# Optimization experiments

Hardware: AMD Instinct MI355X
Metric: run time of the kernel (lower is better)

Reference implementation:

```python
import jax, jax.numpy as jnp
import numpy as np

# Transformer-XL relative multi-head attention (eval mode, dropout = identity)
B, Q, M, D, H = 2, 1024, 1024, 1024, 16
DH = D // H          # 64 head dim
K = Q + M            # key length = memory + current segment
SCALE = 0.02         # param init scale


def setup_inputs() -> dict:
    key = jax.random.key(0)
    ks = jax.random.split(key, 10)
    return {
        "inputs": jax.random.normal(ks[0], (B, Q, D), jnp.float32),
        "inputs_mem": jax.random.normal(ks[1], (B, M, D), jnp.float32),
        "r": jax.random.normal(ks[2], (B, K, D), jnp.float32),
        "W_qkv": jax.random.normal(ks[3], (D, 3 * D), jnp.float32) * SCALE,
        "b_qkv": jnp.zeros((3 * D,), jnp.float32),
        "W_r": jax.random.normal(ks[4], (D, D), jnp.float32) * SCALE,
        "b_r": jnp.zeros((D,), jnp.float32),
        "W_o": jax.random.normal(ks[5], (D, D), jnp.float32) * SCALE,
        "b_o": jnp.zeros((D,), jnp.float32),
        "u": jax.random.normal(ks[6], (1, H, 1, DH), jnp.float32) * SCALE,
        "v": jax.random.normal(ks[7], (1, H, 1, DH), jnp.float32) * SCALE,
    }


def _split_heads(x):
    # [B, L, D] -> [B, H, L, DH]
    b, l, _ = x.shape
    return x.reshape(b, l, H, DH).transpose(0, 2, 1, 3)


def _rel_shift(x):
    # Transformer-XL relative shift: pad one zero column on the left,
    # reshape to [B, H, K+1, Q], drop first row, reshape back.
    b, h, q, k = x.shape
    x = jnp.pad(x, ((0, 0), (0, 0), (0, 0), (1, 0)))
    x = x.reshape(b, h, k + 1, q)[:, :, 1:, :]
    return x.reshape(b, h, q, k)


def reference(inputs, inputs_mem, r, W_qkv, b_qkv, W_r, b_r, W_o, b_o, u, v):
    cat = jnp.concatenate([inputs_mem, inputs], axis=1)      # [B, K, D]
    w = cat @ W_qkv + b_qkv                                   # [B, K, 3D]
    rp = r @ W_r + b_r                                        # [B, K, D]
    # NOTE: source splits as (q, v, k) in that order
    w_q, w_v, w_k = jnp.split(w, 3, axis=-1)
    hq = _split_heads(w_q)[:, :, -Q:]                          # [B, H, Q, DH]
    hk = _split_heads(w_k)                                     # [B, H, K, DH]
    hv = _split_heads(w_v)                                     # [B, H, K, DH]
    hr = _split_heads(rp)                                      # [B, H, K, DH]
    ac = jnp.einsum('bhqd,bhkd->bhqk', hq + u, hk)             # content term
    bd = _rel_shift(jnp.einsum('bhqd,bhkd->bhqk', hq + v, hr)) # position term
    score = (ac + bd) / (DH ** 0.5)
    # causal mask with memory: query i attends to all mem + positions <= i
    mem_len = K - Q
    mask = (jnp.arange(K)[None, :] <= mem_len + jnp.arange(Q)[:, None]).astype(jnp.float32)
    score = score * mask - 1e30 * (1.0 - mask)
    weights = jax.nn.softmax(score, axis=-1)                   # [B, H, Q, K]
    out = jnp.einsum('bhqk,bhkd->bhqd', weights, hv)           # [B, H, Q, DH]
    out = out.transpose(0, 2, 1, 3).reshape(B, Q, D)
    return out @ W_o + b_o
```

## Files before the change

kernel.cpp:

```cpp
#include <hip/hip_runtime.h>
#include <hip/hip_bf16.h>
#include <stdint.h>


typedef __bf16 bf16;
typedef __bf16 bf16x2 __attribute__((ext_vector_type(2)));
typedef __bf16 bf16x4 __attribute__((ext_vector_type(4)));
typedef __bf16 bf16x8 __attribute__((ext_vector_type(8)));
typedef float  f32x4  __attribute__((ext_vector_type(4)));

__device__ __forceinline__ void async_copy16(void* lds, const void* g) {
    auto gp = (const __attribute__((address_space(1))) void*)(uintptr_t)g;
    auto lp = (__attribute__((address_space(3))) void*)(uint32_t)(uintptr_t)lds;
    __builtin_amdgcn_global_load_lds(gp, lp, 16, 0, 0);
}

__device__ __forceinline__ void gemm128_core(
    const bf16* __restrict__ A, const bf16* __restrict__ Bt, const int Kd,
    const int m0, const int n0, bf16* As, bf16* Bs, f32x4 acc[4][4])
{
    const int tid  = threadIdx.x;
    const int lane = tid & 63;
    const int wave = tid >> 6;
    const int wr   = (wave >> 1) * 64;
    const int wc   = (wave & 1) * 64;
    const int lr   = lane & 15;
    const int q4   = lane >> 4;

#pragma unroll
    for (int i = 0; i < 4; ++i)
#pragma unroll
        for (int j = 0; j < 4; ++j) {
            acc[i][j][0] = 0.f; acc[i][j][1] = 0.f; acc[i][j][2] = 0.f; acc[i][j][3] = 0.f;
        }

    auto stage = [&](int buf, int k0) {
#pragma unroll
        for (int it = 0; it < 2; ++it) {
            const int cb0   = (it * 4 + wave) * 64;
            const int chunk = cb0 + lane;
            const int row   = chunk >> 2;
            const int cg    = (chunk & 3) * 8;
            async_copy16(As + buf * 4096 + cb0 * 8, A  + (size_t)(m0 + row) * Kd + k0 + cg);
            async_copy16(Bs + buf * 4096 + cb0 * 8, Bt + (size_t)(n0 + row) * Kd + k0 + cg);
        }
    };

    const int NT = Kd >> 5;
    stage(0, 0);
    __syncthreads();

    for (int t = 0; t < NT; ++t) {
        const int buf = t & 1;
        if (t + 1 < NT) stage(buf ^ 1, (t + 1) * 32);

        const bf16* Ab = As + buf * 4096;
        const bf16* Bb = Bs + buf * 4096;
        bf16x8 af[4], bfr[4];
#pragma unroll
        for (int rb = 0; rb < 4; ++rb)
            af[rb] = *(const bf16x8*)&Ab[(wr + rb * 16 + lr) * 32 + q4 * 8];
#pragma unroll
        for (int cb = 0; cb < 4; ++cb)
            bfr[cb] = *(const bf16x8*)&Bb[(wc + cb * 16 + lr) * 32 + q4 * 8];
#pragma unroll
        for (int rb = 0; rb < 4; ++rb)
#pragma unroll
            for (int cb = 0; cb < 4; ++cb)
                acc[rb][cb] = __builtin_amdgcn_mfma_f32_16x16x32_bf16(af[rb], bfr[cb], acc[rb][cb], 0, 0, 0);
        __syncthreads();
    }
}

__device__ __forceinline__ void gemm64_core(
    const bf16* __restrict__ A, const bf16* __restrict__ Bt, const int Kd,
    const int m0, const int n0, bf16* As, bf16* Bs, f32x4 acc[2][4])
{
    const int tid  = threadIdx.x;
    const int lane = tid & 63;
    const int wave = tid >> 6;
    const int wr   = (wave >> 1) * 32;
    const int wc   = (wave & 1) * 64;
    const int lr   = lane & 15;
    const int q4   = lane >> 4;

#pragma unroll
    for (int i = 0; i < 2; ++i)
#pragma unroll
        for (int j = 0; j < 4; ++j) {
            acc[i][j][0] = 0.f; acc[i][j][1] = 0.f; acc[i][j][2] = 0.f; acc[i][j][3] = 0.f;
        }

    auto stage = [&](int buf, int k0) {
        {
            const int chunk = tid;
            const int row   = chunk >> 2;
            const int cg    = (chunk & 3) * 8;
            async_copy16(As + buf * 2048 + (wave * 64) * 8, A + (size_t)(m0 + row) * Kd + k0 + cg);
        }
#pragma unroll
        for (int it = 0; it < 2; ++it) {
            const int cb0   = (it * 4 + wave) * 64;
            const int chunk = cb0 + lane;
            const int row   = chunk >> 2;
            const int cg    = (chunk & 3) * 8;
            async_copy16(Bs + buf * 4096 + cb0 * 8, Bt + (size_t)(n0 + row) * Kd + k0 + cg);
        }
    };

    const int NT = Kd >> 5;
    stage(0, 0);
    __syncthreads();

    for (int t = 0; t < NT; ++t) {
        const int buf = t & 1;
        if (t + 1 < NT) stage(buf ^ 1, (t + 1) * 32);

        const bf16* Ab = As + buf * 2048;
        const bf16* Bb = Bs + buf * 4096;
        bf16x8 af[2], bfr[4];
#pragma unroll
        for (int rb = 0; rb < 2; ++rb)
            af[rb] = *(const bf16x8*)&Ab[(wr + rb * 16 + lr) * 32 + q4 * 8];
#pragma unroll
        for (int cb = 0; cb < 4; ++cb)
            bfr[cb] = *(const bf16x8*)&Bb[(wc + cb * 16 + lr) * 32 + q4 * 8];
#pragma unroll
        for (int rb = 0; rb < 2; ++rb)
#pragma unroll
            for (int cb = 0; cb < 4; ++cb)
                acc[rb][cb] = __builtin_amdgcn_mfma_f32_16x16x32_bf16(af[rb], bfr[cb], acc[rb][cb], 0, 0, 0);
        __syncthreads();
    }
}

__global__ __launch_bounds__(256) void k_prep(
    const float* __restrict__ Wqkv, const float* __restrict__ Wr,
    const float* __restrict__ Wo,
    const float* __restrict__ mem, const float* __restrict__ inp,
    const float* __restrict__ r,
    bf16* __restrict__ Wqkvt, bf16* __restrict__ Wrt, bf16* __restrict__ Wot,
    bf16* __restrict__ catb, bf16* __restrict__ rb)
{
    __shared__ float t[32][33];
    int id = blockIdx.x;
    if (id < 5120) {
        const float* in; bf16* out; int C, bx, by;
        if (id < 3072)      { in = Wqkv; out = Wqkvt; C = 3072; bx = id % 96; by = id / 96; }
        else if (id < 4096) { id -= 3072; in = Wr; out = Wrt; C = 1024; bx = id & 31; by = id >> 5; }
        else                { id -= 4096; in = Wo; out = Wot; C = 1024; bx = id & 31; by = id >> 5; }
        const int R = 1024;
        const int c0 = bx * 32, r0 = by * 32;
        const int lc = threadIdx.x & 31, lrow = threadIdx.x >> 5;
#pragma unroll
        for (int p = 0; p < 4; ++p)
            t[lrow + p * 8][lc] = in[(size_t)(r0 + lrow + p * 8) * C + c0 + lc];
        __syncthreads();
#pragma unroll
        for (int p = 0; p < 4; ++p)
            out[(size_t)(c0 + lrow + p * 8) * R + r0 + lc] = (bf16)t[lc][lrow + p * 8];
    } else if (id < 9216) {
        const int e   = ((id - 5120) * 256 + threadIdx.x) * 4;
        const int row = e >> 10, dc = e & 1023;
        const int b   = row >> 11, k = row & 2047;
        const float* src = (k < 1024) ? mem + ((size_t)b * 1024 + k) * 1024 + dc
                                      : inp + ((size_t)b * 1024 + (k - 1024)) * 1024 + dc;
        float4 f = *(const float4*)src;
        bf16x4 o; o[0] = (bf16)f.x; o[1] = (bf16)f.y; o[2] = (bf16)f.z; o[3] = (bf16)f.w;
        *(bf16x4*)&catb[e] = o;
    } else {
        const int e = ((id - 9216) * 256 + threadIdx.x) * 4;
        float4 f = *(const float4*)(r + e);
        bf16x4 o; o[0] = (bf16)f.x; o[1] = (bf16)f.y; o[2] = (bf16)f.z; o[3] = (bf16)f.w;
        *(bf16x4*)&rb[e] = o;
    }
}

__global__ __launch_bounds__(256) void k_gemm_qkvr(
    const bf16* __restrict__ catb, const bf16* __restrict__ Wqkvt,
    const float* __restrict__ b_qkv, const float* __restrict__ u, const float* __restrict__ v,
    const bf16* __restrict__ rb_, const bf16* __restrict__ Wrt,
    const float* __restrict__ b_r,
    bf16* __restrict__ hq_u, bf16* __restrict__ hq_v,
    bf16* __restrict__ hk, bf16* __restrict__ hvT, bf16* __restrict__ hr)
{
    __shared__ bf16 lds[4 * 128 * 32];
    f32x4 acc[4][4];
    const int lane = threadIdx.x & 63, wave = threadIdx.x >> 6;
    const int wr = (wave >> 1) * 64, wc = (wave & 1) * 64;
    const int lr = lane & 15, q4 = lane >> 4;
    const int y = blockIdx.y;

    if (y < 16) {
        const int m0 = blockIdx.x * 128;
        const int n0 = 1024 + y * 128;
        gemm128_core(catb, Wqkvt, 1024, m0, n0, lds, lds + 2 * 4096, acc);
#pragma unroll
        for (int rb = 0; rb < 4; ++rb) {
#pragma unroll
            for (int cb = 0; cb < 4; ++cb) {
                const int col  = n0 + wc + cb * 16 + lr;
                const int part = col >> 10;
                const int hd   = col & 1023;
                const int h    = hd >> 6, d = hd & 63;
                const float bcol = b_qkv[col];
#pragma unroll
                for (int r = 0; r < 4; ++r) {
                    const int row = m0 + wr + rb * 16 + q4 * 4 + r;
                    const int b   = row >> 11, k = row & 2047;
                    const float val = acc[rb][cb][r] + bcol;
                    if (part == 1) {
                        const int ks = (k & ~63) | ((k & 63) ^ ((d & 7) << 3));
                        hvT[(((size_t)(b * 16 + h)) * 64 + d) * 2048 + ks] = (bf16)val;
                    } else {
                        const int ds = d ^ ((k & 7) << 3);
                        hk[(((size_t)(b * 16 + h)) * 2048 + k) * 64 + ds] = (bf16)val;
                    }
                }
            }
        }
    } else if (y < 20) {
        const int linear = (y - 16) * 32 + blockIdx.x;
        const int n0 = (linear & 7) * 128;
        const int mi = linear >> 3;
        const int m0 = (mi >> 3) * 2048 + 1024 + (mi & 7) * 128;
        gemm128_core(catb, Wqkvt, 1024, m0, n0, lds, lds + 2 * 4096, acc);
#pragma unroll
        for (int rb = 0; rb < 4; ++rb) {
#pragma unroll
            for (int cb = 0; cb < 4; ++cb) {
                const int col = n0 + wc + cb * 16 + lr;
                const int h = col >> 6, d = col & 63;
                const float bcol = b_qkv[col];
                const float uc = u[col], vc = v[col];
#pragma unroll
                for (int r = 0; r < 4; ++r) {
                    const int row = m0 + wr + rb * 16 + q4 * 4 + r;
                    const int b   = row >> 11, k = row & 2047;
                    const float val = acc[rb][cb][r] + bcol;
                    const size_t o = (((size_t)(b * 16 + h)) * 1024 + (k - 1024)) * 64 + d;
                    hq_u[o] = (bf16)(val + uc);
                    hq_v[o] = (bf16)(val + vc);
                }
            }
        }
    } else {
        const int m0 = blockIdx.x * 128;
        const int n0 = (y - 20) * 128;
        gemm128_core(rb_, Wrt, 1024, m0, n0, lds, lds + 2 * 4096, acc);
#pragma unroll
        for (int rb = 0; rb < 4; ++rb) {
#pragma unroll
            for (int cb = 0; cb < 4; ++cb) {
                const int col = n0 + wc + cb * 16 + lr;
                const int h = col >> 6, d = col & 63;
                const float bcol = b_r[col];
#pragma unroll
                for (int r = 0; r < 4; ++r) {
                    const int row = m0 + wr + rb * 16 + q4 * 4 + r;
                    const int b = row >> 11, k = row & 2047;
                    const int ds = d ^ ((k & 7) << 3);
                    hr[(((size_t)(b * 16 + h)) * 2048 + k) * 64 + ds] = (bf16)(acc[rb][cb][r] + bcol);
                }
            }
        }
    }
}

__global__ __launch_bounds__(256) void k_gemm_out(
    const bf16* __restrict__ attn, const bf16* __restrict__ Wt,
    const float* __restrict__ bias, float* __restrict__ out)
{
    __shared__ bf16 lds[2 * 2048 + 2 * 4096];
    f32x4 acc[2][4];
    const int m0 = blockIdx.x * 64, n0 = blockIdx.y * 128;
    gemm64_core(attn, Wt, 1024, m0, n0, lds, lds + 2 * 2048, acc);

    const int lane = threadIdx.x & 63, wave = threadIdx.x >> 6;
    const int wr = (wave >> 1) * 32, wc = (wave & 1) * 64;
    const int lr = lane & 15, q4 = lane >> 4;
#pragma unroll
    for (int rb = 0; rb < 2; ++rb) {
#pragma unroll
        for (int cb = 0; cb < 4; ++cb) {
            const int col = n0 + wc + cb * 16 + lr;
            const float bcol = bias[col];
#pragma unroll
            for (int r = 0; r < 4; ++r) {
                const int row = m0 + wr + rb * 16 + q4 * 4 + r;
                out[(size_t)row * 1024 + col] = acc[rb][cb][r] + bcol;
            }
        }
    }
}

__global__ __launch_bounds__(256) void k_attn(
    const bf16* __restrict__ hq_u, const bf16* __restrict__ hq_v,
    const bf16* __restrict__ hk, const bf16* __restrict__ hvT,
    const bf16* __restrict__ hr, bf16* __restrict__ attn)
{
    __shared__ bf16 Ks[2][64][64];
    __shared__ bf16 Vt[2][64][64];
    __shared__ bf16 Rs[192][64];
    __shared__ bf16 U[4][1600];

    const int bh = blockIdx.y;
    const int qt = (bh & 16) ? (15 - (int)blockIdx.x) : (int)blockIdx.x;
    const int q0 = qt * 64;
    const int tid = threadIdx.x, lane = tid & 63, wave = tid >> 6;
    const int lr = lane & 15, q4 = lane >> 4;
    bf16* Uw = &U[wave][0];

    const int nt  = 17 + qt;
    const int m0c = 15 - qt;
    const size_t kvbase = (size_t)bh * 2048 * 64;

    const int r0_ = tid >> 3, c0_ = (tid & 7) * 8;
    const int r1_ = 32 + r0_, c1_ = c0_;

    auto stage_kv = [&](int t, int buf) {
        const int k0 = t * 64;
        async_copy16(&Ks[buf][r0_][c0_], &hk [kvbase + (size_t)(k0 + r0_) * 64 + c0_]);
        async_copy16(&Ks[buf][r1_][c1_], &hk [kvbase + (size_t)(k0 + r1_) * 64 + c1_]);
        async_copy16(&Vt[buf][r0_][c0_], &hvT[kvbase + (size_t)r0_ * 2048 + k0 + c0_]);
        async_copy16(&Vt[buf][r1_][c1_], &hvT[kvbase + (size_t)r1_ * 2048 + k0 + c1_]);
    };
    auto stage_r = [&](int c, int slot) {
        if (c * 64 < 2048) {
            async_copy16(&Rs[slot * 64 + r0_][c0_], &hr[kvbase + (size_t)(c * 64 + r0_) * 64 + c0_]);
            async_copy16(&Rs[slot * 64 + r1_][c1_], &hr[kvbase + (size_t)(c * 64 + r1_) * 64 + c1_]);
        }
    };

    const size_t qrow = ((size_t)bh * 1024 + q0 + wave * 16 + lr) * 64;
    const bf16x8 qu0 = *(const bf16x8*)&hq_u[qrow + q4 * 8];
    const bf16x8 qu1 = *(const bf16x8*)&hq_u[qrow + 32 + q4 * 8];
    const bf16x8 qv0 = *(const bf16x8*)&hq_v[qrow + q4 * 8];
    const bf16x8 qv1 = *(const bf16x8*)&hq_v[qrow + 32 + q4 * 8];

    const int sw  = (lr & 7) << 3;
    const int cA0 = (q4 * 8) ^ sw;
    const int cA1 = (32 + q4 * 8) ^ sw;

    f32x4 Oacc[4];
#pragma unroll
    for (int i = 0; i < 4; ++i) { Oacc[i][0] = 0.f; Oacc[i][1] = 0.f; Oacc[i][2] = 0.f; Oacc[i][3] = 0.f; }
    float lp[4] = {0.f, 0.f, 0.f, 0.f};

    stage_kv(0, 0);
    stage_r(m0c,     m0c % 3);
    stage_r(m0c + 1, (m0c + 1) % 3);
    __syncthreads();

    for (int t = 0; t < nt; ++t) {
        const int k0  = t * 64;
        const int mt  = m0c + t;
        const int s0  = mt % 3;
        const int s1  = (s0 + 1 == 3) ? 0 : s0 + 1;
        const int s2  = (s1 + 1 == 3) ? 0 : s1 + 1;
        const int buf = t & 1;
        const bool more = (t + 1 < nt);
        if (more) { stage_kv(t + 1, buf ^ 1); stage_r(mt + 2, s2); }

        __builtin_amdgcn_s_setprio(1);
        f32x4 S[4];
#pragma unroll
        for (int cb = 0; cb < 4; ++cb) {
            const bf16x8 kf0 = *(const bf16x8*)&Ks[buf][cb * 16 + lr][cA0];
            const bf16x8 kf1 = *(const bf16x8*)&Ks[buf][cb * 16 + lr][cA1];
            f32x4 z; z[0] = 0.f; z[1] = 0.f; z[2] = 0.f; z[3] = 0.f;
            z = __builtin_amdgcn_mfma_f32_16x16x32_bf16(qu0, kf0, z, 0, 0, 0);
            S[cb] = __builtin_amdgcn_mfma_f32_16x16x32_bf16(qu1, kf1, z, 0, 0, 0);
        }
#pragma unroll
        for (int jbi = 0; jbi < 5; ++jbi) {
            const int jb   = jbi + 3 - wave;
            const int rrow = ((jb & 4) ? s1 : s0) * 64 + (jb & 3) * 16 + lr;
            const bf16x8 rf0 = *(const bf16x8*)&Rs[rrow][cA0];
            const bf16x8 rf1 = *(const bf16x8*)&Rs[rrow][cA1];
            f32x4 z; z[0] = 0.f; z[1] = 0.f; z[2] = 0.f; z[3] = 0.f;
            z = __builtin_amdgcn_mfma_f32_16x16x32_bf16(qv0, rf0, z, 0, 0, 0);
            z = __builtin_amdgcn_mfma_f32_16x16x32_bf16(qv1, rf1, z, 0, 0, 0);
            bf16x4 pk;
            pk[0] = (bf16)z[0]; pk[1] = (bf16)z[1]; pk[2] = (bf16)z[2]; pk[3] = (bf16)z[3];
            *(bf16x4*)&Uw[(jbi * 16 + lr) * 20 + q4 * 4] = pk;
        }

        float bdv[4][4];
#pragma unroll
        for (int cb = 0; cb < 4; ++cb)
#pragma unroll
            for (int r = 0; r < 4; ++r) {
                const int tq = q4 * 4 + r;
                bdv[cb][r] = (float)Uw[(cb * 16 + lr + 15 - tq) * 20 + tq];
            }

#pragma unroll
        for (int cb = 0; cb < 4; ++cb) {
            const int k = k0 + cb * 16 + lr;
#pragma unroll
            for (int r = 0; r < 4; ++r) {
                const int q = q0 + wave * 16 + q4 * 4 + r;
                const float s = (S[cb][r] + bdv[cb][r]) * 0.125f;
                const float p = (k <= 1024 + q) ? __expf(s) : 0.f;
                lp[r] += p;
                Uw[(q4 * 4 + r) * 76 + cb * 16 + lr] = (bf16)p;
            }
        }

        const bf16x8 pf0 = *(const bf16x8*)&Uw[lr * 76 + q4 * 8];
        const bf16x8 pf1 = *(const bf16x8*)&Uw[lr * 76 + 32 + q4 * 8];
#pragma unroll
        for (int db = 0; db < 4; ++db) {
            const bf16x8 vf0 = *(const bf16x8*)&Vt[buf][db * 16 + lr][cA0];
            const bf16x8 vf1 = *(const bf16x8*)&Vt[buf][db * 16 + lr][cA1];
            Oacc[db] = __builtin_amdgcn_mfma_f32_16x16x32_bf16(pf0, vf0, Oacc[db], 0, 0, 0);
            Oacc[db] = __builtin_amdgcn_mfma_f32_16x16x32_bf16(pf1, vf1, Oacc[db], 0, 0, 0);
        }
        __builtin_amdgcn_s_setprio(0);

        if (more) __syncthreads();
    }

#pragma unroll
    for (int off = 1; off < 16; off <<= 1)
#pragma unroll
        for (int r = 0; r < 4; ++r) lp[r] += __shfl_xor(lp[r], off, 64);

    const int b = bh >> 4, h = bh & 15;
#pragma unroll
    for (int r = 0; r < 4; ++r) {
        const float rl = 1.f / lp[r];
        const int q = q0 + wave * 16 + q4 * 4 + r;
#pragma unroll
        for (int db = 0; db < 4; ++db) {
            const int d = db * 16 + lr;
            attn[(((size_t)b * 1024 + q) * 16 + h) * 64 + d] = (bf16)(Oacc[db][r] * rl);
        }
    }
}

extern "C" void kernel_launch(void* const* d_in, const int* in_sizes, int n_in,
                              void* d_out, int out_size, void* d_ws, size_t ws_size,
                              hipStream_t stream)
{
    const float* inputs = (const float*)d_in[0];
    const float* mem    = (const float*)d_in[1];
    const float* r      = (const float*)d_in[2];
    const float* W_qkv  = (const float*)d_in[3];
    const float* b_qkv  = (const float*)d_in[4];
    const float* W_r    = (const float*)d_in[5];
    const float* b_r    = (const float*)d_in[6];
    const float* W_o    = (const float*)d_in[7];
    const float* b_o    = (const float*)d_in[8];
    const float* u      = (const float*)d_in[9];
    const float* v      = (const float*)d_in[10];
    float* out = (float*)d_out;

    char* ws = (char*)d_ws;
    size_t off = 0;
    auto alloc = [&](size_t bytes) -> void* {
        void* p = ws + off;
        off += (bytes + 255) & ~(size_t)255;
        return p;
    };
    bf16* hq_u  = (bf16*)alloc(2ull * 16 * 1024 * 64 * 2);
    bf16* hq_v  = (bf16*)alloc(2ull * 16 * 1024 * 64 * 2);
    bf16* hk    = (bf16*)alloc(2ull * 16 * 2048 * 64 * 2);
    bf16* hvT   = (bf16*)alloc(2ull * 16 * 2048 * 64 * 2);
    bf16* hr    = (bf16*)alloc(2ull * 16 * 2048 * 64 * 2);
    bf16* attnb = (bf16*)alloc(2ull * 1024 * 1024 * 2);
    bf16* Wot   = (bf16*)alloc(1024ull * 1024 * 2);
    bf16* catb  = (bf16*)alloc(4096ull * 1024 * 2);
    bf16* rb    = (bf16*)alloc(4096ull * 1024 * 2);
    bf16* Wqkvt = (bf16*)alloc(3072ull * 1024 * 2);
    bf16* Wrt   = (bf16*)alloc(1024ull * 1024 * 2);

    k_prep<<<13312, 256, 0, stream>>>(W_qkv, W_r, W_o, mem, inputs, r,
                                      Wqkvt, Wrt, Wot, catb, rb);

    k_gemm_qkvr<<<dim3(32, 28), 256, 0, stream>>>(catb, Wqkvt, b_qkv, u, v,
                                                  rb, Wrt, b_r,
                                                  hq_u, hq_v, hk, hvT, hr);
    k_attn<<<dim3(16, 32), 256, 0, stream>>>(hq_u, hq_v, hk, hvT, hr, attnb);
    k_gemm_out<<<dim3(32, 8), 256, 0, stream>>>(attnb, Wot, b_o, out);
}
```

Measured before the change: 243.5 us.

## Software-pipeline PV matmul one tile behind QK in attention kernel

Defers each tile's P·V MFMA to the next iteration, so the softmax exp/LDS writes of the current tile can overlap with the previous tile's PV MFMAs. V staging moves to a triple buffer so the lagging tile's V stays resident, and P fragments are kept in registers across iterations. This costs extra LDS (one more V tile) and more register pressure, and adds an epilogue step for the final tile.

```diff
diff --git a/kernel.cpp b/kernel.cpp
--- a/kernel.cpp
+++ b/kernel.cpp
@@ -300,7 +300,7 @@
     const bf16* __restrict__ hr, bf16* __restrict__ attn)
 {
     __shared__ bf16 Ks[2][64][64];
-    __shared__ bf16 Vt[2][64][64];
+    __shared__ bf16 Vt[3][64][64];
     __shared__ bf16 Rs[192][64];
     __shared__ bf16 U[4][1600];
 
@@ -318,12 +318,15 @@
     const int r0_ = tid >> 3, c0_ = (tid & 7) * 8;
     const int r1_ = 32 + r0_, c1_ = c0_;
 
-    auto stage_kv = [&](int t, int buf) {
+    auto stage_k = [&](int t, int buf) {
         const int k0 = t * 64;
-        async_copy16(&Ks[buf][r0_][c0_], &hk [kvbase + (size_t)(k0 + r0_) * 64 + c0_]);
-        async_copy16(&Ks[buf][r1_][c1_], &hk [kvbase + (size_t)(k0 + r1_) * 64 + c1_]);
-        async_copy16(&Vt[buf][r0_][c0_], &hvT[kvbase + (size_t)r0_ * 2048 + k0 + c0_]);
-        async_copy16(&Vt[buf][r1_][c1_], &hvT[kvbase + (size_t)r1_ * 2048 + k0 + c1_]);
+        async_copy16(&Ks[buf][r0_][c0_], &hk[kvbase + (size_t)(k0 + r0_) * 64 + c0_]);
+        async_copy16(&Ks[buf][r1_][c1_], &hk[kvbase + (size_t)(k0 + r1_) * 64 + c1_]);
+    };
+    auto stage_v = [&](int t, int slot) {
+        const int k0 = t * 64;
+        async_copy16(&Vt[slot][r0_][c0_], &hvT[kvbase + (size_t)r0_ * 2048 + k0 + c0_]);
+        async_copy16(&Vt[slot][r1_][c1_], &hvT[kvbase + (size_t)r1_ * 2048 + k0 + c1_]);
     };
     auto stage_r = [&](int c, int slot) {
         if (c * 64 < 2048) {
@@ -346,8 +349,10 @@
 #pragma unroll
     for (int i = 0; i < 4; ++i) { Oacc[i][0] = 0.f; Oacc[i][1] = 0.f; Oacc[i][2] = 0.f; Oacc[i][3] = 0.f; }
     float lp[4] = {0.f, 0.f, 0.f, 0.f};
-
-    stage_kv(0, 0);
+    bf16x8 pf0p, pf1p;
+
+    stage_k(0, 0);
+    stage_v(0, 0);
     stage_r(m0c,     m0c % 3);
     stage_r(m0c + 1, (m0c + 1) % 3);
     __syncthreads();
@@ -360,7 +365,11 @@
         const int s2  = (s1 + 1 == 3) ? 0 : s1 + 1;
         const int buf = t & 1;
         const bool more = (t + 1 < nt);
-        if (more) { stage_kv(t + 1, buf ^ 1); stage_r(mt + 2, s2); }
+        if (more) {
+            stage_k(t + 1, buf ^ 1);
+            stage_v(t + 1, (t + 1) % 3);
+            stage_r(mt + 2, s2);
+        }
 
         __builtin_amdgcn_s_setprio(1);
         f32x4 S[4];
@@ -408,18 +417,35 @@
             }
         }
 
-        const bf16x8 pf0 = *(const bf16x8*)&Uw[lr * 76 + q4 * 8];
-        const bf16x8 pf1 = *(const bf16x8*)&Uw[lr * 76 + 32 + q4 * 8];
+        const bf16x8 pf0n = *(const bf16x8*)&Uw[lr * 76 + q4 * 8];
+        const bf16x8 pf1n = *(const bf16x8*)&Uw[lr * 76 + 32 + q4 * 8];
+
+        if (t > 0) {
+            const int vs = (t - 1) % 3;
+#pragma unroll
+            for (int db = 0; db < 4; ++db) {
+                const bf16x8 vf0 = *(const bf16x8*)&Vt[vs][db * 16 + lr][cA0];
+                const bf16x8 vf1 = *(const bf16x8*)&Vt[vs][db * 16 + lr][cA1];
+                Oacc[db] = __builtin_amdgcn_mfma_f32_16x16x32_bf16(pf0p, vf0, Oacc[db], 0, 0, 0);
+                Oacc[db] = __builtin_amdgcn_mfma_f32_16x16x32_bf16(pf1p, vf1, Oacc[db], 0, 0, 0);
+            }
+        }
+        __builtin_amdgcn_s_setprio(0);
+
+        pf0p = pf0n; pf1p = pf1n;
+
+        if (more) __syncthreads();
+    }
+
+    {
+        const int vs = (nt - 1) % 3;
 #pragma unroll
         for (int db = 0; db < 4; ++db) {
-            const bf16x8 vf0 = *(const bf16x8*)&Vt[buf][db * 16 + lr][cA0];
-            const bf16x8 vf1 = *(const bf16x8*)&Vt[buf][db * 16 + lr][cA1];
-            Oacc[db] = __builtin_amdgcn_mfma_f32_16x16x32_bf16(pf0, vf0, Oacc[db], 0, 0, 0);
-            Oacc[db] = __builtin_amdgcn_mfma_f32_16x16x32_bf16(pf1, vf1, Oacc[db], 0, 0, 0);
-        }
-        __builtin_amdgcn_s_setprio(0);
-
-        if (more) __syncthreads();
+            const bf16x8 vf0 = *(const bf16x8*)&Vt[vs][db * 16 + lr][cA0];
+            const bf16x8 vf1 = *(const bf16x8*)&Vt[vs][db * 16 + lr][cA1];
+            Oacc[db] = __builtin_amdgcn_mfma_f32_16x16x32_bf16(pf0p, vf0, Oacc[db], 0, 0, 0);
+            Oacc[db] = __builtin_amdgcn_mfma_f32_16x16x32_bf16(pf1p, vf1, Oacc[db], 0, 0, 0);
+        }
     }
 
 #pragma unroll
```

After: 249.4 us. 1.02x slower.

## Split attention KV range across two blocks and combine partials in new kernel

Applied to the files above, without the earlier changes.

Splits each attention block's key-tile loop into two halves handled by separate blocks (grid doubles to 1024 blocks), writing unnormalized fp32 partial outputs and row sums, then adds a combine kernel that sums and normalizes. It also replaces the async global-to-LDS double-buffered staging with register prefetch plus single-buffered LDS writes behind two barriers. The aim is better CU occupancy and load balance for the causal triangle. The cost is extra partial-result traffic, an extra launch, and more synchronization per tile. Scratch buffers are reused for the partials.

```diff
diff --git a/kernel.cpp b/kernel.cpp
--- a/kernel.cpp
+++ b/kernel.cpp
@@ -297,14 +297,17 @@
 __global__ __launch_bounds__(256) void k_attn(
     const bf16* __restrict__ hq_u, const bf16* __restrict__ hq_v,
     const bf16* __restrict__ hk, const bf16* __restrict__ hvT,
-    const bf16* __restrict__ hr, bf16* __restrict__ attn)
-{
-    __shared__ bf16 Ks[2][64][64];
-    __shared__ bf16 Vt[2][64][64];
-    __shared__ bf16 Rs[192][64];
+    const bf16* __restrict__ hr,
+    float* __restrict__ partO, float* __restrict__ partl)
+{
+    __shared__ bf16 Ks[64][64];
+    __shared__ bf16 Vt[64][64];
+    __shared__ bf16 Rs[128][64];
     __shared__ bf16 U[4][1600];
 
-    const int bh = blockIdx.y;
+    const int ybl  = blockIdx.y;
+    const int pair = ybl >> 5;
+    const int bh   = ybl & 31;
     const int qt = (bh & 16) ? (15 - (int)blockIdx.x) : (int)blockIdx.x;
     const int q0 = qt * 64;
     const int tid = threadIdx.x, lane = tid & 63, wave = tid >> 6;
@@ -312,24 +315,41 @@
     bf16* Uw = &U[wave][0];
 
     const int nt  = 17 + qt;
+    const int h0  = (nt + 1) >> 1;
+    const int t0  = pair ? h0 : 0;
+    const int t1  = pair ? nt : h0;
     const int m0c = 15 - qt;
     const size_t kvbase = (size_t)bh * 2048 * 64;
 
     const int r0_ = tid >> 3, c0_ = (tid & 7) * 8;
-    const int r1_ = 32 + r0_, c1_ = c0_;
-
-    auto stage_kv = [&](int t, int buf) {
+    const int r1_ = 32 + r0_;
+
+    bf16x8 kv0, kv1, vv0, vv1, rv0, rv1;
+    auto load_kv = [&](int t) {
         const int k0 = t * 64;
-        async_copy16(&Ks[buf][r0_][c0_], &hk [kvbase + (size_t)(k0 + r0_) * 64 + c0_]);
-        async_copy16(&Ks[buf][r1_][c1_], &hk [kvbase + (size_t)(k0 + r1_) * 64 + c1_]);
-        async_copy16(&Vt[buf][r0_][c0_], &hvT[kvbase + (size_t)r0_ * 2048 + k0 + c0_]);
-        async_copy16(&Vt[buf][r1_][c1_], &hvT[kvbase + (size_t)r1_ * 2048 + k0 + c1_]);
-    };
-    auto stage_r = [&](int c, int slot) {
+        kv0 = *(const bf16x8*)&hk [kvbase + (size_t)(k0 + r0_) * 64 + c0_];
+        kv1 = *(const bf16x8*)&hk [kvbase + (size_t)(k0 + r1_) * 64 + c0_];
+        vv0 = *(const bf16x8*)&hvT[kvbase + (size_t)r0_ * 2048 + k0 + c0_];
+        vv1 = *(const bf16x8*)&hvT[kvbase + (size_t)r1_ * 2048 + k0 + c0_];
+    };
+    auto load_r = [&](int c) {
         if (c * 64 < 2048) {
-            async_copy16(&Rs[slot * 64 + r0_][c0_], &hr[kvbase + (size_t)(c * 64 + r0_) * 64 + c0_]);
-            async_copy16(&Rs[slot * 64 + r1_][c1_], &hr[kvbase + (size_t)(c * 64 + r1_) * 64 + c1_]);
-        }
+            rv0 = *(const bf16x8*)&hr[kvbase + (size_t)(c * 64 + r0_) * 64 + c0_];
+            rv1 = *(const bf16x8*)&hr[kvbase + (size_t)(c * 64 + r1_) * 64 + c0_];
+        } else {
+#pragma unroll
+            for (int z = 0; z < 8; ++z) { rv0[z] = (bf16)0.f; rv1[z] = (bf16)0.f; }
+        }
+    };
+    auto write_kv = [&]() {
+        *(bf16x8*)&Ks[r0_][c0_] = kv0;
+        *(bf16x8*)&Ks[r1_][c0_] = kv1;
+        *(bf16x8*)&Vt[r0_][c0_] = vv0;
+        *(bf16x8*)&Vt[r1_][c0_] = vv1;
+    };
+    auto write_r = [&](int slot) {
+        *(bf16x8*)&Rs[slot * 64 + r0_][c0_] = rv0;
+        *(bf16x8*)&Rs[slot * 64 + r1_][c0_] = rv1;
     };
 
     const size_t qrow = ((size_t)bh * 1024 + q0 + wave * 16 + lr) * 64;
@@ -347,27 +367,26 @@
     for (int i = 0; i < 4; ++i) { Oacc[i][0] = 0.f; Oacc[i][1] = 0.f; Oacc[i][2] = 0.f; Oacc[i][3] = 0.f; }
     float lp[4] = {0.f, 0.f, 0.f, 0.f};
 
-    stage_kv(0, 0);
-    stage_r(m0c,     m0c % 3);
-    stage_r(m0c + 1, (m0c + 1) % 3);
+    {
+        const int c0c = m0c + t0;
+        load_kv(t0); write_kv();
+        load_r(c0c);     write_r(c0c & 1);
+        load_r(c0c + 1); write_r((c0c + 1) & 1);
+    }
     __syncthreads();
 
-    for (int t = 0; t < nt; ++t) {
-        const int k0  = t * 64;
-        const int mt  = m0c + t;
-        const int s0  = mt % 3;
-        const int s1  = (s0 + 1 == 3) ? 0 : s0 + 1;
-        const int s2  = (s1 + 1 == 3) ? 0 : s1 + 1;
-        const int buf = t & 1;
-        const bool more = (t + 1 < nt);
-        if (more) { stage_kv(t + 1, buf ^ 1); stage_r(mt + 2, s2); }
+    for (int t = t0; t < t1; ++t) {
+        const int k0 = t * 64;
+        const int mt = m0c + t;
+        const bool more = (t + 1 < t1);
+        if (more) { load_kv(t + 1); load_r(mt + 2); }
 
         __builtin_amdgcn_s_setprio(1);
         f32x4 S[4];
 #pragma unroll
         for (int cb = 0; cb < 4; ++cb) {
-            const bf16x8 kf0 = *(const bf16x8*)&Ks[buf][cb * 16 + lr][cA0];
-            const bf16x8 kf1 = *(const bf16x8*)&Ks[buf][cb * 16 + lr][cA1];
+            const bf16x8 kf0 = *(const bf16x8*)&Ks[cb * 16 + lr][cA0];
+            const bf16x8 kf1 = *(const bf16x8*)&Ks[cb * 16 + lr][cA1];
             f32x4 z; z[0] = 0.f; z[1] = 0.f; z[2] = 0.f; z[3] = 0.f;
             z = __builtin_amdgcn_mfma_f32_16x16x32_bf16(qu0, kf0, z, 0, 0, 0);
             S[cb] = __builtin_amdgcn_mfma_f32_16x16x32_bf16(qu1, kf1, z, 0, 0, 0);
@@ -375,7 +394,7 @@
 #pragma unroll
         for (int jbi = 0; jbi < 5; ++jbi) {
             const int jb   = jbi + 3 - wave;
-            const int rrow = ((jb & 4) ? s1 : s0) * 64 + (jb & 3) * 16 + lr;
+            const int rrow = (((jb & 4) ? (mt + 1) : mt) & 1) * 64 + (jb & 3) * 16 + lr;
             const bf16x8 rf0 = *(const bf16x8*)&Rs[rrow][cA0];
             const bf16x8 rf1 = *(const bf16x8*)&Rs[rrow][cA1];
             f32x4 z; z[0] = 0.f; z[1] = 0.f; z[2] = 0.f; z[3] = 0.f;
@@ -412,14 +431,19 @@
         const bf16x8 pf1 = *(const bf16x8*)&Uw[lr * 76 + 32 + q4 * 8];
 #pragma unroll
         for (int db = 0; db < 4; ++db) {
-            const bf16x8 vf0 = *(const bf16x8*)&Vt[buf][db * 16 + lr][cA0];
-            const bf16x8 vf1 = *(const bf16x8*)&Vt[buf][db * 16 + lr][cA1];
+            const bf16x8 vf0 = *(const bf16x8*)&Vt[db * 16 + lr][cA0];
+            const bf16x8 vf1 = *(const bf16x8*)&Vt[db * 16 + lr][cA1];
             Oacc[db] = __builtin_amdgcn_mfma_f32_16x16x32_bf16(pf0, vf0, Oacc[db], 0, 0, 0);
             Oacc[db] = __builtin_amdgcn_mfma_f32_16x16x32_bf16(pf1, vf1, Oacc[db], 0, 0, 0);
         }
         __builtin_amdgcn_s_setprio(0);
 
-        if (more) __syncthreads();
+        if (more) {
+            __syncthreads();
+            write_kv();
+            write_r((mt + 2) & 1);
+            __syncthreads();
+        }
     }
 
 #pragma unroll
@@ -427,17 +451,39 @@
 #pragma unroll
         for (int r = 0; r < 4; ++r) lp[r] += __shfl_xor(lp[r], off, 64);
 
+    const size_t pbase = ((size_t)(pair * 512 + bh * 16 + qt)) * 64;
+#pragma unroll
+    for (int r = 0; r < 4; ++r) {
+        const int lq = wave * 16 + q4 * 4 + r;
+        if (lr == 0) partl[pbase + lq] = lp[r];
+#pragma unroll
+        for (int db = 0; db < 4; ++db)
+            partO[(pbase + lq) * 64 + db * 16 + lr] = Oacc[db][r];
+    }
+}
+
+__global__ __launch_bounds__(256) void k_comb(
+    const float* __restrict__ partO, const float* __restrict__ partl,
+    bf16* __restrict__ attnb)
+{
+    const int idx = blockIdx.x * 256 + threadIdx.x;
+    const int e   = idx * 4;
+    const int d    = e & 63;
+    const int lq   = (e >> 6) & 63;
+    const int bhqt = e >> 12;
+    const float4 a = *(const float4*)&partO[((size_t)bhqt * 64 + lq) * 64 + d];
+    const float4 c = *(const float4*)&partO[((size_t)(512 + bhqt) * 64 + lq) * 64 + d];
+    const float l  = partl[bhqt * 64 + lq] + partl[512 * 64 + bhqt * 64 + lq];
+    const float rl = 1.f / l;
+    const int bh = bhqt >> 4, qt = bhqt & 15;
     const int b = bh >> 4, h = bh & 15;
-#pragma unroll
-    for (int r = 0; r < 4; ++r) {
-        const float rl = 1.f / lp[r];
-        const int q = q0 + wave * 16 + q4 * 4 + r;
-#pragma unroll
-        for (int db = 0; db < 4; ++db) {
-            const int d = db * 16 + lr;
-            attn[(((size_t)b * 1024 + q) * 16 + h) * 64 + d] = (bf16)(Oacc[db][r] * rl);
-        }
-    }
+    const int q = qt * 64 + lq;
+    bf16x4 o;
+    o[0] = (bf16)((a.x + c.x) * rl);
+    o[1] = (bf16)((a.y + c.y) * rl);
+    o[2] = (bf16)((a.z + c.z) * rl);
+    o[3] = (bf16)((a.w + c.w) * rl);
+    *(bf16x4*)&attnb[(((size_t)b * 1024 + q) * 16 + h) * 64 + d] = o;
 }
 
 extern "C" void kernel_launch(void* const* d_in, const int* in_sizes, int n_in,
@@ -476,12 +522,16 @@
     bf16* Wqkvt = (bf16*)alloc(3072ull * 1024 * 2);
     bf16* Wrt   = (bf16*)alloc(1024ull * 1024 * 2);
 
+    float* partO = (float*)catb;
+    float* partl = (float*)Wqkvt;
+
     k_prep<<<13312, 256, 0, stream>>>(W_qkv, W_r, W_o, mem, inputs, r,
                                       Wqkvt, Wrt, Wot, catb, rb);
 
     k_gemm_qkvr<<<dim3(32, 28), 256, 0, stream>>>(catb, Wqkvt, b_qkv, u, v,
                                                   rb, Wrt, b_r,
                                                   hq_u, hq_v, hk, hvT, hr);
-    k_attn<<<dim3(16, 32), 256, 0, stream>>>(hq_u, hq_v, hk, hvT, hr, attnb);
+    k_attn<<<dim3(16, 64), 256, 0, stream>>>(hq_u, hq_v, hk, hvT, hr, partO, partl);
+    k_comb<<<2048, 256, 0, stream>>>(partO, partl, attnb);
     k_gemm_out<<<dim3(32, 8), 256, 0, stream>>>(attnb, Wot, b_o, out);
 }
```

New measurement: 255.5 us. 4.9% more time.
